# Kernel tuning notes

Hardware: AMD Instinct MI355X
Metric: run time of the kernel (lower is better)

The kernel has to match this reference:

```python
import jax, jax.numpy as jnp
import numpy as np

N, E, IN, HID, H, OUT = 50000, 800000, 128, 64, 4, 128
NEG = 0.2   # LeakyReLU slope in GATv2
EPS = 1e-5  # BatchNorm eps


def _seg_softmax(a, seg, n):
    # numerically stable softmax over edges grouped by destination node
    amax = jax.lax.stop_gradient(jax.ops.segment_max(a, seg, num_segments=n))
    amax = jnp.where(jnp.isfinite(amax), amax, 0.0)
    ex = jnp.exp(a - amax[seg])
    den = jax.ops.segment_sum(ex, seg, num_segments=n)
    return ex / (den[seg] + 1e-16)


def _gatv2(x, src, dst, e_attr, Wl, bl, Wr, br, We, att, bias, heads, c, concat):
    n = x.shape[0]
    xl = (x @ Wl + bl).reshape(n, heads, c)   # source transform (x_j)
    xr = (x @ Wr + br).reshape(n, heads, c)   # target transform (x_i)
    ee = (e_attr @ We).reshape(-1, heads, c)  # edge feature transform
    m = xl[src] + xr[dst] + ee                # [E, H, C]
    m = jnp.where(m > 0, m, NEG * m)          # LeakyReLU
    alpha = _seg_softmax(jnp.einsum('ehc,hc->eh', m, att), dst, n)  # [E, H]
    out = jax.ops.segment_sum(alpha[:, :, None] * xl[src], dst, num_segments=n)
    out = out.reshape(n, heads * c) if concat else out.mean(axis=1)
    return out + bias


def _bn(h, g, b):  # BatchNorm1d, training-mode batch stats (biased var)
    mu = jnp.mean(h, axis=0)
    var = jnp.var(h, axis=0)
    return (h - mu) * jax.lax.rsqrt(var + EPS) * g + b


def _prelu(h, a):
    return jnp.where(h > 0, h, a * h)


def setup_inputs() -> dict:
    key = jax.random.key(0)
    ks = jax.random.split(key, 16)
    def nrm(k, shape, fan):
        return jax.random.normal(k, shape, jnp.float32) / np.float32(np.sqrt(fan))
    x = jax.random.normal(ks[0], (N, IN), jnp.float32)
    edge_index = jax.random.randint(ks[1], (2, E), 0, N, jnp.int32)
    edge_attr = jax.random.uniform(ks[2], (E, 1), dtype=jnp.float32)
    return {
        'x': x, 'edge_index': edge_index, 'edge_attr': edge_attr,
        # layer 1: heads=4, concat=True
        'Wl1': nrm(ks[3], (IN, H * HID), IN), 'bl1': jnp.zeros((H * HID,), jnp.float32),
        'Wr1': nrm(ks[4], (IN, H * HID), IN), 'br1': jnp.zeros((H * HID,), jnp.float32),
        'We1': nrm(ks[5], (1, H * HID), 1),
        'att1': nrm(ks[6], (H, HID), HID),
        'cb1': jnp.zeros((H * HID,), jnp.float32),
        'bng1': jnp.ones((H * HID,), jnp.float32), 'bnb1': jnp.zeros((H * HID,), jnp.float32),
        'pa': jnp.float32(0.25),  # PReLU single parameter (shared by both uses)
        # layer 2: heads=1, concat=False
        'Wl2': nrm(ks[7], (H * HID, OUT), H * HID), 'bl2': jnp.zeros((OUT,), jnp.float32),
        'Wr2': nrm(ks[8], (H * HID, OUT), H * HID), 'br2': jnp.zeros((OUT,), jnp.float32),
        'We2': nrm(ks[9], (1, OUT), 1),
        'att2': nrm(ks[10], (1, OUT), OUT),
        'cb2': jnp.zeros((OUT,), jnp.float32),
        'bng2': jnp.ones((OUT,), jnp.float32), 'bnb2': jnp.zeros((OUT,), jnp.float32),
        'skipW': nrm(ks[11], (IN, OUT), IN), 'skipb': jnp.zeros((OUT,), jnp.float32),
    }


def reference(x, edge_index, edge_attr, Wl1, bl1, Wr1, br1, We1, att1, cb1,
              bng1, bnb1, pa, Wl2, bl2, Wr2, br2, We2, att2, cb2, bng2, bnb2,
              skipW, skipb):
    src, dst = edge_index[0], edge_index[1]
    h = _gatv2(x, src, dst, edge_attr, Wl1, bl1, Wr1, br1, We1, att1, cb1, H, HID, True)
    h = _prelu(_bn(h, bng1, bnb1), pa)  # dropout = identity (eval)
    h = _gatv2(h, src, dst, edge_attr, Wl2, bl2, Wr2, br2, We2, att2, cb2, 1, OUT, False)
    h = _prelu(_bn(h, bng2, bnb2), pa)
    return h + (x @ skipW + skipb)
```

## Files before the change

kernel.cpp:

```cpp
#include <hip/hip_runtime.h>
#include <cstdint>
#include <cstddef>

#define NNODES 50000
#define NEDGES 800000
#define DH1    256
#define DOUT   128

typedef unsigned short u16;
typedef __bf16 bf16x8 __attribute__((ext_vector_type(8)));
typedef float  f32x4  __attribute__((ext_vector_type(4)));

__device__ __forceinline__ float bf2f(unsigned int u) {
  union { unsigned int i; float f; } x; x.i = u << 16; return x.f;
}
__device__ __forceinline__ u16 f2bf(float f) {
  union { float f; unsigned int i; } x; x.f = f;
  unsigned int r = x.i + 0x7fffu + ((x.i >> 16) & 1u);
  return (u16)(r >> 16);
}
__device__ __forceinline__ void dec8(uint4 r, float* o) {
  o[0] = bf2f(r.x & 0xffffu); o[1] = bf2f(r.x >> 16);
  o[2] = bf2f(r.y & 0xffffu); o[3] = bf2f(r.y >> 16);
  o[4] = bf2f(r.z & 0xffffu); o[5] = bf2f(r.z >> 16);
  o[6] = bf2f(r.w & 0xffffu); o[7] = bf2f(r.w >> 16);
}
__device__ __forceinline__ uint4 pack8(const float* v) {
  uint4 p;
  p.x = (unsigned)f2bf(v[0]) | ((unsigned)f2bf(v[1]) << 16);
  p.y = (unsigned)f2bf(v[2]) | ((unsigned)f2bf(v[3]) << 16);
  p.z = (unsigned)f2bf(v[4]) | ((unsigned)f2bf(v[5]) << 16);
  p.w = (unsigned)f2bf(v[6]) | ((unsigned)f2bf(v[7]) << 16);
  return p;
}
template<int IMM>
__device__ __forceinline__ float swz(float v) {
  return __int_as_float(__builtin_amdgcn_ds_swizzle(__float_as_int(v), IMM));
}


#define CNT_BLKS 3125
#define CVT_BLKS 6250
#define W1_BLKS  320
#define W2_BLKS  256

__global__ __launch_bounds__(256) void setup_k(
    const int* __restrict__ dst, int* __restrict__ cnt, int* __restrict__ rank,
    const float* __restrict__ x, u16* __restrict__ xbf,
    const float* __restrict__ Wl1, const float* __restrict__ Wr1,
    const float* __restrict__ bl1, const float* __restrict__ br1,
    const float* __restrict__ Wl2, const float* __restrict__ Wr2,
    const float* __restrict__ bl2, const float* __restrict__ br2,
    const float* __restrict__ skW, const float* __restrict__ skb,
    const float* __restrict__ att1, const float* __restrict__ We1,
    const float* __restrict__ att2, const float* __restrict__ We2,
    u16* __restrict__ Wcat1, float* __restrict__ bias1,
    u16* __restrict__ Wt2, float* __restrict__ bias2,
    float* __restrict__ axw, int2* __restrict__ epair) {
  int b = blockIdx.x, t = threadIdx.x;
  if (b < CNT_BLKS) {
    int e = b * 256 + t;
    if (e < NEDGES) rank[e] = atomicAdd(&cnt[dst[e]], 1);
  } else if (b < CNT_BLKS + CVT_BLKS) {
    int i = ((b - CNT_BLKS) * 256 + t) * 4;
    float4 v = *reinterpret_cast<const float4*>(x + i);
    uint2 pk;
    pk.x = (unsigned)f2bf(v.x) | ((unsigned)f2bf(v.y) << 16);
    pk.y = (unsigned)f2bf(v.z) | ((unsigned)f2bf(v.w) << 16);
    *reinterpret_cast<uint2*>(xbf + i) = pk;
  } else if (b < CNT_BLKS + CVT_BLKS + W1_BLKS) {
    int idx = (b - CNT_BLKS - CVT_BLKS) * 256 + t;
    if (idx < 640) bias1[idx] = idx < 256 ? bl1[idx] : idx < 512 ? br1[idx - 256] : skb[idx - 512];
    int n = idx >> 7, k = idx & 127;
    float v = n < 256 ? Wl1[k * 256 + n] : n < 512 ? Wr1[k * 256 + (n - 256)] : skW[k * 128 + (n - 512)];
    Wcat1[idx] = f2bf(v);
  } else if (b < CNT_BLKS + CVT_BLKS + W1_BLKS + W2_BLKS) {
    int idx = (b - CNT_BLKS - CVT_BLKS - W1_BLKS) * 256 + t;
    if (idx < 256) bias2[idx] = idx < 128 ? bl2[idx] : br2[idx - 128];
    int n = idx >> 8, k = idx & 255;
    float v = n < 128 ? Wl2[k * 128 + n] : Wr2[k * 128 + (n - 128)];
    Wt2[idx] = f2bf(v);
  } else if (b == CNT_BLKS + CVT_BLKS + W1_BLKS + W2_BLKS) {
    if (t < 4) {
      float s = 0.f;
      for (int c = 0; c < 64; ++c) s += att1[t * 64 + c] * We1[t * 64 + c];
      axw[t] = s;
    } else if (t == 4) {
      float s = 0.f;
      for (int c = 0; c < 128; ++c) s += att2[c] * We2[c];
      axw[4] = s;
    }
  } else {
    int2 z; z.x = 0; z.y = 0;
    epair[NEDGES + t] = z;
  }
}


__global__ __launch_bounds__(256) void offsets_k(const int* __restrict__ cnt, int* __restrict__ offs,
                                                 int* __restrict__ total) {
  int i = blockIdx.x * 256 + threadIdx.x;
  int lane = threadIdx.x & 63;
  int c = (i < NNODES) ? cnt[i] : 0;
  int incl = c;
  #pragma unroll
  for (int d = 1; d < 64; d <<= 1) {
    int t = __shfl_up(incl, d, 64);
    if (lane >= d) incl += t;
  }
  int wtotal = __shfl(incl, 63, 64);
  int base = 0;
  if (lane == 63) base = atomicAdd(total, wtotal);
  base = __shfl(base, 63, 64);
  int off = base + incl - c;
  if (i < NNODES) offs[i] = off;
}

__global__ __launch_bounds__(256) void scatter_k(const int* __restrict__ src, const int* __restrict__ dst,
                                                 const float* __restrict__ ea, const int* __restrict__ offs,
                                                 const int* __restrict__ rank, int2* __restrict__ epair) {
  int e = blockIdx.x * 256 + threadIdx.x;
  if (e >= NEDGES) return;
  int p = offs[dst[e]] + rank[e];
  int2 v; v.x = src[e]; v.y = __float_as_int(ea[e]);
  epair[p] = v;
}


template<int K, int NPASS, int B1, int B2, int LDC0, int LDC1, int LDC2,
         int SPAN, int ATTLEN, bool DO_ATT, bool FUSE_BN>
__global__ __launch_bounds__(512) void gemm_fused(
    const u16* __restrict__ A, const u16* __restrict__ Wt, const float* __restrict__ bias,
    u16* __restrict__ C0, u16* __restrict__ C1, u16* __restrict__ C2,
    const float* __restrict__ att, float* __restrict__ axl, float* __restrict__ axr,
    const float* __restrict__ bnsum, const float* __restrict__ bnsq,
    const float* __restrict__ bng, const float* __restrict__ bnb,
    const float* __restrict__ pap) {
  constexpr int LDA = K + 8;
  constexpr int CSTR = 136;
  __shared__ __align__(16) u16 As[64 * LDA];
  __shared__ __align__(16) u16 Cs[64 * CSTR];
  __shared__ float attS[128];
  __shared__ float scS[K], shS[K];
  const int tid = threadIdx.x;
  const int row0 = blockIdx.x * 64;

  if constexpr (FUSE_BN) {
    if (tid < K) {
      const float invN = 1.0f / (float)NNODES;
      float mu = bnsum[tid] * invN;
      float var = bnsq[tid] * invN - mu * mu;
      float s = bng[tid] * rsqrtf(var + 1e-5f);
      scS[tid] = s;
      shS[tid] = bnb[tid] - mu * s;
    }
    __syncthreads();
  }
  const float pa = FUSE_BN ? pap[0] : 0.f;
  #pragma unroll
  for (int it = 0; it < K / 32; ++it) {
    int chunk = it * 512 + tid;
    int row = chunk / (K / 4);
    int col = (chunk % (K / 4)) * 4;
    uint2 v; v.x = 0u; v.y = 0u;
    int gr = row0 + row;
    if (gr < NNODES) v = *reinterpret_cast<const uint2*>(A + (size_t)gr * K + col);
    if constexpr (FUSE_BN) {
      float o0 = bf2f(v.x & 0xffffu) * scS[col]     + shS[col];
      float o1 = bf2f(v.x >> 16)     * scS[col + 1] + shS[col + 1];
      float o2 = bf2f(v.y & 0xffffu) * scS[col + 2] + shS[col + 2];
      float o3 = bf2f(v.y >> 16)     * scS[col + 3] + shS[col + 3];
      o0 = o0 > 0.f ? o0 : pa * o0;
      o1 = o1 > 0.f ? o1 : pa * o1;
      o2 = o2 > 0.f ? o2 : pa * o2;
      o3 = o3 > 0.f ? o3 : pa * o3;
      v.x = (unsigned)f2bf(o0) | ((unsigned)f2bf(o1) << 16);
      v.y = (unsigned)f2bf(o2) | ((unsigned)f2bf(o3) << 16);
    }
    *reinterpret_cast<uint2*>(&As[row * LDA + col]) = v;
  }
  __syncthreads();

  const int w = tid >> 6, lane = tid & 63, q = lane >> 4, l16 = lane & 15;
  const int tc = w * 16 + l16;

  #pragma unroll
  for (int p = 0; p < NPASS; ++p) {
    const int cb = p * 128;
    const int ncol = cb + tc;
    f32x4 acc[4];
    #pragma unroll
    for (int rt = 0; rt < 4; ++rt) acc[rt] = (f32x4){0.f, 0.f, 0.f, 0.f};
    const u16* wp = Wt + (size_t)ncol * K + q * 8;
    #pragma unroll
    for (int ks = 0; ks < K / 32; ++ks) {
      bf16x8 b = *reinterpret_cast<const bf16x8*>(wp + ks * 32);
      #pragma unroll
      for (int rt = 0; rt < 4; ++rt) {
        bf16x8 a = *reinterpret_cast<const bf16x8*>(&As[(rt * 16 + l16) * LDA + ks * 32 + q * 8]);
        acc[rt] = __builtin_amdgcn_mfma_f32_16x16x32_bf16(a, b, acc[rt], 0, 0, 0);
      }
    }
    const float bval = bias[ncol];
    #pragma unroll
    for (int rt = 0; rt < 4; ++rt)
      #pragma unroll
      for (int r = 0; r < 4; ++r)
        Cs[(rt * 16 + q * 4 + r) * CSTR + tc] = f2bf(acc[rt][r] + bval);
    if (DO_ATT && cb < B2 && tid < 128) attS[tid] = att[(cb + tid) % ATTLEN];
    __syncthreads();
    {
      u16* Cg; int LD, cc;
      if (cb < B1)      { Cg = C0; LD = LDC0; cc = cb; }
      else if (cb < B2) { Cg = C1; LD = LDC1; cc = cb - B1; }
      else              { Cg = C2; LD = LDC2; cc = cb - B2; }
      #pragma unroll
      for (int it = 0; it < 2; ++it) {
        int ch = it * 512 + tid;
        int row = ch / 16, co = (ch % 16) * 8;
        int grow = row0 + row;
        if (grow < NNODES) {
          uint4 v = *reinterpret_cast<const uint4*>(&Cs[row * CSTR + co]);
          *reinterpret_cast<uint4*>(Cg + (size_t)grow * LD + cc + co) = v;
        }
      }
    }
    if constexpr (DO_ATT) {
      if (cb < B2) {
        constexpr int TPU = SPAN / 16;
        constexpr int HIT = 128 / SPAN;
        constexpr int HEADS = B1 / SPAN;
        int unit = tid / TPU, sub = tid % TPU;
        int row = unit / HIT, hb = unit % HIT;
        int c0 = hb * SPAN + sub * 16;
        float s = 0.f;
        #pragma unroll
        for (int c = 0; c < 16; ++c)
          s += bf2f(Cs[row * CSTR + c0 + c]) * attS[c0 + c];
        #pragma unroll
        for (int d = 1; d < TPU; d <<= 1) s += __shfl_xor(s, d, 64);
        int grow = row0 + row;
        if (sub == 0 && grow < NNODES) {
          int cbl = cb < B1 ? cb : cb - B1;
          int head = cbl / SPAN + hb;
          float* dstp = (cb < B1) ? axl : axr;
          dstp[grow * HEADS + head] = s;
        }
      }
    }
    __syncthreads();
  }
}


template<int HEADS, int CHAN, int EPW>
__global__ __launch_bounds__(256) void gat_edge(
    const int* __restrict__ offs, const int* __restrict__ cnt,
    const int2* __restrict__ epair,
    const u16* __restrict__ xl, const u16* __restrict__ xr,
    const float* __restrict__ att, const float* __restrict__ We,
    const float* __restrict__ cb,
    const float* __restrict__ axl, const float* __restrict__ axr,
    const float* __restrict__ aWep, u16* __restrict__ hout) {
  constexpr int HC  = HEADS * CHAN;
  constexpr int GSZ = 64 / EPW;
  constexpr int CPL = HC / GSZ;
  constexpr int LPH = CHAN / CPL;
  static_assert(CPL == 8, "layout");

  int node = __builtin_amdgcn_readfirstlane((int)(blockIdx.x * 4 + (threadIdx.x >> 6)));
  if (node >= NNODES) return;
  const int lane = threadIdx.x & 63;
  const int g    = lane / GSZ;
  const int lgs  = lane & (GSZ - 1);
  const int h    = lgs / LPH;
  const int cbase = lgs * CPL;

  float xrv[8], attv[8], wev[8];
  {
    uint4 xrr = *reinterpret_cast<const uint4*>(xr + (size_t)node * HC + cbase);
    dec8(xrr, xrv);
    float4 a0 = *reinterpret_cast<const float4*>(att + cbase);
    float4 a1 = *reinterpret_cast<const float4*>(att + cbase + 4);
    float4 w0 = *reinterpret_cast<const float4*>(We + cbase);
    float4 w1 = *reinterpret_cast<const float4*>(We + cbase + 4);
    attv[0]=a0.x; attv[1]=a0.y; attv[2]=a0.z; attv[3]=a0.w;
    attv[4]=a1.x; attv[5]=a1.y; attv[6]=a1.z; attv[7]=a1.w;
    wev[0]=w0.x; wev[1]=w0.y; wev[2]=w0.z; wev[3]=w0.w;
    wev[4]=w1.x; wev[5]=w1.y; wev[6]=w1.z; wev[7]=w1.w;
  }
  const float aWe = aWep[h];
  const float axr_n = axr[node * HEADS + h];
  const int off = __builtin_amdgcn_readfirstlane(offs[node]);
  const int deg = __builtin_amdgcn_readfirstlane(cnt[node]);

  float den = 0.f;
  float accv[8];
  #pragma unroll
  for (int c = 0; c < 8; ++c) accv[c] = 0.f;

  {
    const int last = deg - 1;
    const int2* pp = epair + off + g;
    int2 p_cur = pp[0];
    int2 p_nxt = pp[EPW];
    uint4 r_cur; float ax_cur;
    { int s = p_cur.x;
      r_cur = *reinterpret_cast<const uint4*>(xl + (size_t)s * HC + cbase);
      ax_cur = axl[s * HEADS + h]; }
    const int niter = (deg + EPW - 1) / EPW;
    for (int i = 0; i < niter; ++i) {
      int2 p_n2 = pp[(i + 2) * EPW];
      uint4 r_n; float ax_n;
      { int s = p_nxt.x;
        r_n = *reinterpret_cast<const uint4*>(xl + (size_t)s * HC + cbase);
        ax_n = axl[s * HEADS + h]; }
      float ea = __int_as_float(p_cur.y);
      float xlv[8];
      dec8(r_cur, xlv);
      float part2 = 0.f;
      #pragma unroll
      for (int c = 0; c < 8; ++c) {
        float m = xlv[c] + fmaf(ea, wev[c], xrv[c]);
        part2 = fmaf(fabsf(m), attv[c], part2);
      }
      if constexpr (LPH >= 2)  part2 += swz<0x041F>(part2);
      if constexpr (LPH >= 4)  part2 += swz<0x081F>(part2);
      if constexpr (LPH >= 8)  part2 += swz<0x101F>(part2);
      if constexpr (LPH >= 16) part2 += swz<0x201F>(part2);
      float ssum = ax_cur + fmaf(ea, aWe, axr_n);
      float sc = fmaf(0.4f, part2, 0.6f * ssum);
      float e = __expf(sc);
      e = (i * EPW + g <= last) ? e : 0.f;
      den += e;
      #pragma unroll
      for (int c = 0; c < 8; ++c) accv[c] = fmaf(e, xlv[c], accv[c]);
      p_cur = p_nxt; p_nxt = p_n2; r_cur = r_n; ax_cur = ax_n;
    }
  }
  #pragma unroll
  for (int d = GSZ; d < 64; d <<= 1) {
    den += __shfl_xor(den, d, 64);
    #pragma unroll
    for (int c = 0; c < 8; ++c) accv[c] += __shfl_xor(accv[c], d, 64);
  }
  if (g == 0) {
    float inv = 1.0f / (den + 1e-16f);
    float4 c0 = *reinterpret_cast<const float4*>(cb + cbase);
    float4 c1 = *reinterpret_cast<const float4*>(cb + cbase + 4);
    float ov[8];
    ov[0] = accv[0] * inv + c0.x; ov[1] = accv[1] * inv + c0.y;
    ov[2] = accv[2] * inv + c0.z; ov[3] = accv[3] * inv + c0.w;
    ov[4] = accv[4] * inv + c1.x; ov[5] = accv[5] * inv + c1.y;
    ov[6] = accv[6] * inv + c1.z; ov[7] = accv[7] * inv + c1.w;
    *reinterpret_cast<uint4*>(hout + (size_t)node * HC + cbase) = pack8(ov);
  }
}


template<int NC>
__global__ void bn_stats_bf(const u16* __restrict__ h, float* __restrict__ sum, float* __restrict__ sq) {
  int c = threadIdx.x;
  float s = 0.f, q = 0.f;
  for (int r = blockIdx.x; r < NNODES; r += gridDim.x) {
    float v = bf2f(h[(size_t)r * NC + c]);
    s += v; q += v * v;
  }
  atomicAdd(&sum[c], s);
  atomicAdd(&sq[c], q);
}

__global__ __launch_bounds__(256) void final_out_k(
    const u16* __restrict__ h2, const u16* __restrict__ skip,
    const float* __restrict__ sum, const float* __restrict__ sq,
    const float* __restrict__ g, const float* __restrict__ bb_,
    const float* __restrict__ pap, float* __restrict__ outp, int total) {
  int i = (blockIdx.x * 256 + threadIdx.x) * 4;
  if (i >= total) return;
  const float invN = 1.0f / (float)NNODES;
  float pa = pap[0];
  int c = i & 127;
  float4 sm = *reinterpret_cast<const float4*>(sum + c);
  float4 qq = *reinterpret_cast<const float4*>(sq + c);
  float4 gg = *reinterpret_cast<const float4*>(g + c);
  float4 bb = *reinterpret_cast<const float4*>(bb_ + c);
  float mu, var, sc[4], sh[4];
  mu = sm.x * invN; var = qq.x * invN - mu * mu; sc[0] = gg.x * rsqrtf(var + 1e-5f); sh[0] = bb.x - mu * sc[0];
  mu = sm.y * invN; var = qq.y * invN - mu * mu; sc[1] = gg.y * rsqrtf(var + 1e-5f); sh[1] = bb.y - mu * sc[1];
  mu = sm.z * invN; var = qq.z * invN - mu * mu; sc[2] = gg.z * rsqrtf(var + 1e-5f); sh[2] = bb.z - mu * sc[2];
  mu = sm.w * invN; var = qq.w * invN - mu * mu; sc[3] = gg.w * rsqrtf(var + 1e-5f); sh[3] = bb.w - mu * sc[3];
  uint2 raw = *reinterpret_cast<const uint2*>(h2 + i);
  float v0 = bf2f(raw.x & 0xffffu), v1 = bf2f(raw.x >> 16);
  float v2 = bf2f(raw.y & 0xffffu), v3 = bf2f(raw.y >> 16);
  uint2 skr = *reinterpret_cast<const uint2*>(skip + i);
  float s0 = bf2f(skr.x & 0xffffu), s1 = bf2f(skr.x >> 16);
  float s2 = bf2f(skr.y & 0xffffu), s3 = bf2f(skr.y >> 16);
  float4 o;
  o.x = v0 * sc[0] + sh[0]; o.x = (o.x > 0.f ? o.x : pa * o.x) + s0;
  o.y = v1 * sc[1] + sh[1]; o.y = (o.y > 0.f ? o.y : pa * o.y) + s1;
  o.z = v2 * sc[2] + sh[2]; o.z = (o.z > 0.f ? o.z : pa * o.z) + s2;
  o.w = v3 * sc[3] + sh[3]; o.w = (o.w > 0.f ? o.w : pa * o.w) + s3;
  *reinterpret_cast<float4*>(outp + i) = o;
}


extern "C" void kernel_launch(void* const* d_in, const int* in_sizes, int n_in,
                              void* d_out, int out_size, void* d_ws, size_t ws_size,
                              hipStream_t stream) {
  (void)in_sizes; (void)n_in; (void)out_size; (void)ws_size;
  const float* x    = (const float*)d_in[0];
  const int*   ei   = (const int*)d_in[1];
  const float* ea   = (const float*)d_in[2];
  const float* Wl1  = (const float*)d_in[3];
  const float* bl1  = (const float*)d_in[4];
  const float* Wr1  = (const float*)d_in[5];
  const float* br1  = (const float*)d_in[6];
  const float* We1  = (const float*)d_in[7];
  const float* att1 = (const float*)d_in[8];
  const float* cb1  = (const float*)d_in[9];
  const float* bng1 = (const float*)d_in[10];
  const float* bnb1 = (const float*)d_in[11];
  const float* pa   = (const float*)d_in[12];
  const float* Wl2  = (const float*)d_in[13];
  const float* bl2  = (const float*)d_in[14];
  const float* Wr2  = (const float*)d_in[15];
  const float* br2  = (const float*)d_in[16];
  const float* We2  = (const float*)d_in[17];
  const float* att2 = (const float*)d_in[18];
  const float* cb2  = (const float*)d_in[19];
  const float* bng2 = (const float*)d_in[20];
  const float* bnb2 = (const float*)d_in[21];
  const float* skW  = (const float*)d_in[22];
  const float* skb  = (const float*)d_in[23];
  const int* srcp = ei;
  const int* dstp = ei + NEDGES;

  char* base = (char*)d_ws;
  size_t off = 0;
  auto alloc = [&](size_t bytes) -> char* {
    char* p = base + off;
    off = (off + bytes + 255) & ~(size_t)255;
    return p;
  };
  size_t zero_ints = 1 + NNODES + 256 + 256 + 128 + 128;
  char* zbase = alloc(zero_ints * 4);
  int*   totalp = (int*)zbase;
  int*   cnt    = totalp + 1;
  float* bnsum1 = (float*)(cnt + NNODES);
  float* bnsq1  = bnsum1 + 256;
  float* bnsum2 = bnsq1 + 256;
  float* bnsq2  = bnsum2 + 128;

  int*   offs    = (int*)alloc((size_t)NNODES * 4);
  int*   rank    = (int*)alloc((size_t)NEDGES * 4);
  int2*  epair   = (int2*)alloc(((size_t)NEDGES + 256) * 8);
  const size_t RBYTES = (size_t)NNODES * DH1 * 2;
  char* regionA = alloc(RBYTES);
  char* regionB = alloc(RBYTES);
  char* regionC = alloc(RBYTES);
  u16*   xbf    = (u16*)alloc((size_t)NNODES * 128 * 2);
  u16*   skipbf = (u16*)alloc((size_t)NNODES * 128 * 2);
  u16*   Wcat1  = (u16*)alloc(640 * 128 * 2);
  u16*   Wt2    = (u16*)alloc(256 * 256 * 2);
  float* bias1  = (float*)alloc(640 * 4);
  float* bias2  = (float*)alloc(256 * 4);
  float* axw    = (float*)alloc(8 * 4);
  float* axl1   = (float*)alloc((size_t)NNODES * 4 * 4);
  float* axr1   = (float*)alloc((size_t)NNODES * 4 * 4);
  float* axl2   = (float*)alloc((size_t)NNODES * 4);
  float* axr2   = (float*)alloc((size_t)NNODES * 4);

  u16*   xl1     = (u16*)regionA;
  u16*   xr1     = (u16*)regionB;
  u16*   h1      = (u16*)regionC;
  u16*   xl2     = (u16*)regionB;
  u16*   xr2     = (u16*)(regionB + (size_t)NNODES * DOUT * 2);
  u16*   h2      = (u16*)regionA;

  hipMemsetAsync(zbase, 0, zero_ints * 4, stream);

  const int EB = (NEDGES + 255) / 256;
  const int NB = (NNODES + 255) / 256;
  setup_k<<<CNT_BLKS + CVT_BLKS + W1_BLKS + W2_BLKS + 2, 256, 0, stream>>>(
      dstp, cnt, rank, x, xbf, Wl1, Wr1, bl1, br1, Wl2, Wr2, bl2, br2, skW, skb,
      att1, We1, att2, We2, Wcat1, bias1, Wt2, bias2, axw, epair);
  offsets_k<<<NB, 256, 0, stream>>>(cnt, offs, totalp);
  scatter_k<<<EB, 256, 0, stream>>>(srcp, dstp, ea, offs, rank, epair);

  const int MB64 = (NNODES + 63) / 64;
  gemm_fused<128, 5, 256, 512, 256, 256, 128, 64, 256, true, false><<<MB64, 512, 0, stream>>>(
      xbf, Wcat1, bias1, xl1, xr1, skipbf, att1, axl1, axr1,
      (const float*)0, (const float*)0, (const float*)0, (const float*)0, (const float*)0);
  gat_edge<4, 64, 2><<<(NNODES + 3) / 4, 256, 0, stream>>>(
      offs, cnt, epair, xl1, xr1, att1, We1, cb1, axl1, axr1, axw, h1);
  bn_stats_bf<256><<<800, 256, 0, stream>>>(h1, bnsum1, bnsq1);

  gemm_fused<256, 2, 128, 256, 128, 128, 1, 128, 128, true, true><<<MB64, 512, 0, stream>>>(
      h1, Wt2, bias2, xl2, xr2, (u16*)0, att2, axl2, axr2,
      bnsum1, bnsq1, bng1, bnb1, pa);
  gat_edge<1, 128, 4><<<(NNODES + 3) / 4, 256, 0, stream>>>(
      offs, cnt, epair, xl2, xr2, att2, We2, cb2, axl2, axr2, axw + 4, h2);
  bn_stats_bf<128><<<800, 128, 0, stream>>>(h2, bnsum2, bnsq2);
  final_out_k<<<(NNODES * DOUT / 4 + 255) / 256, 256, 0, stream>>>(
      h2, skipbf, bnsum2, bnsq2, bng2, bnb2, pa, (float*)d_out, NNODES * DOUT);
}
```

Baseline: 447.2 us.

## Fold softmax constants into exp2, use DPP reductions, deepen edge prefetch

The 0.6·log2(e) and 0.4·log2(e) factors of the rewritten LeakyReLU score are now folded into the precomputed axl/axr/axw values and the attention vector. The edge loop can then call a raw exp2 with no extra multiplies. The cross-lane partial-sum reduction switches from ds_swizzle to DPP adds, which avoids the LDS-path latency. Source-row gathers are prefetched two edges ahead instead of one, using 32-bit byte offsets, and the tail mask is checked only on the last iteration. The deeper prefetch costs extra registers.

After: 439.5 us. About the same (-1.7%).

```diff
diff --git a/kernel.cpp b/kernel.cpp
--- a/kernel.cpp
+++ b/kernel.cpp
@@ -6,6 +6,9 @@
 #define NEDGES 800000
 #define DH1    256
 #define DOUT   128
+
+#define K1F 0.8656170245333781f
+#define K2F 0.5770780163555854f
 
 typedef unsigned short u16;
 typedef __bf16 bf16x8 __attribute__((ext_vector_type(8)));
@@ -33,9 +36,17 @@
   p.w = (unsigned)f2bf(v[6]) | ((unsigned)f2bf(v[7]) << 16);
   return p;
 }
-template<int IMM>
-__device__ __forceinline__ float swz(float v) {
-  return __int_as_float(__builtin_amdgcn_ds_swizzle(__float_as_int(v), IMM));
+template<int CTRL>
+__device__ __forceinline__ float dppadd(float v) {
+  int t = __builtin_amdgcn_update_dpp(0, __float_as_int(v), CTRL, 0xF, 0xF, true);
+  return v + __int_as_float(t);
+}
+__device__ __forceinline__ float fexp2(float x) {
+#if __has_builtin(__builtin_amdgcn_exp2f)
+  return __builtin_amdgcn_exp2f(x);
+#else
+  return exp2f(x);
+#endif
 }
 
 
@@ -84,11 +95,11 @@
     if (t < 4) {
       float s = 0.f;
       for (int c = 0; c < 64; ++c) s += att1[t * 64 + c] * We1[t * 64 + c];
-      axw[t] = s;
+      axw[t] = s * K1F;
     } else if (t == 4) {
       float s = 0.f;
       for (int c = 0; c < 128; ++c) s += att2[c] * We2[c];
-      axw[4] = s;
+      axw[4] = s * K1F;
     }
   } else {
     int2 z; z.x = 0; z.y = 0;
@@ -244,7 +255,7 @@
           int cbl = cb < B1 ? cb : cb - B1;
           int head = cbl / SPAN + hb;
           float* dstp = (cb < B1) ? axl : axr;
-          dstp[grow * HEADS + head] = s;
+          dstp[grow * HEADS + head] = s * K1F;
         }
       }
     }
@@ -284,8 +295,8 @@
     float4 a1 = *reinterpret_cast<const float4*>(att + cbase + 4);
     float4 w0 = *reinterpret_cast<const float4*>(We + cbase);
     float4 w1 = *reinterpret_cast<const float4*>(We + cbase + 4);
-    attv[0]=a0.x; attv[1]=a0.y; attv[2]=a0.z; attv[3]=a0.w;
-    attv[4]=a1.x; attv[5]=a1.y; attv[6]=a1.z; attv[7]=a1.w;
+    attv[0]=a0.x*K2F; attv[1]=a0.y*K2F; attv[2]=a0.z*K2F; attv[3]=a0.w*K2F;
+    attv[4]=a1.x*K2F; attv[5]=a1.y*K2F; attv[6]=a1.z*K2F; attv[7]=a1.w*K2F;
     wev[0]=w0.x; wev[1]=w0.y; wev[2]=w0.z; wev[3]=w0.w;
     wev[4]=w1.x; wev[5]=w1.y; wev[6]=w1.z; wev[7]=w1.w;
   }
@@ -294,49 +305,58 @@
   const int off = __builtin_amdgcn_readfirstlane(offs[node]);
   const int deg = __builtin_amdgcn_readfirstlane(cnt[node]);
 
+  const char* __restrict__ xlb  = (const char*)xl;
+  const char* __restrict__ axlb = (const char*)axl;
+  const unsigned cboff = (unsigned)(cbase * 2);
+  const unsigned hoff  = (unsigned)(h * 4);
+
   float den = 0.f;
   float accv[8];
   #pragma unroll
   for (int c = 0; c < 8; ++c) accv[c] = 0.f;
 
+  const int niter = (deg + EPW - 1) / EPW;
+  const int2* pp = epair + off + g;
+  int2 p0 = pp[0];
+  int2 p1 = pp[EPW];
+  int2 p2 = pp[2 * EPW];
+  uint4 r0, r1; float ax0, ax1;
   {
-    const int last = deg - 1;
-    const int2* pp = epair + off + g;
-    int2 p_cur = pp[0];
-    int2 p_nxt = pp[EPW];
-    uint4 r_cur; float ax_cur;
-    { int s = p_cur.x;
-      r_cur = *reinterpret_cast<const uint4*>(xl + (size_t)s * HC + cbase);
-      ax_cur = axl[s * HEADS + h]; }
-    const int niter = (deg + EPW - 1) / EPW;
-    for (int i = 0; i < niter; ++i) {
-      int2 p_n2 = pp[(i + 2) * EPW];
-      uint4 r_n; float ax_n;
-      { int s = p_nxt.x;
-        r_n = *reinterpret_cast<const uint4*>(xl + (size_t)s * HC + cbase);
-        ax_n = axl[s * HEADS + h]; }
-      float ea = __int_as_float(p_cur.y);
-      float xlv[8];
-      dec8(r_cur, xlv);
-      float part2 = 0.f;
-      #pragma unroll
-      for (int c = 0; c < 8; ++c) {
-        float m = xlv[c] + fmaf(ea, wev[c], xrv[c]);
-        part2 = fmaf(fabsf(m), attv[c], part2);
-      }
-      if constexpr (LPH >= 2)  part2 += swz<0x041F>(part2);
-      if constexpr (LPH >= 4)  part2 += swz<0x081F>(part2);
-      if constexpr (LPH >= 8)  part2 += swz<0x101F>(part2);
-      if constexpr (LPH >= 16) part2 += swz<0x201F>(part2);
-      float ssum = ax_cur + fmaf(ea, aWe, axr_n);
-      float sc = fmaf(0.4f, part2, 0.6f * ssum);
-      float e = __expf(sc);
-      e = (i * EPW + g <= last) ? e : 0.f;
-      den += e;
-      #pragma unroll
-      for (int c = 0; c < 8; ++c) accv[c] = fmaf(e, xlv[c], accv[c]);
-      p_cur = p_nxt; p_nxt = p_n2; r_cur = r_n; ax_cur = ax_n;
-    }
+    unsigned b0 = (unsigned)p0.x * (unsigned)(HC * 2) + cboff;
+    r0  = *reinterpret_cast<const uint4*>(xlb + b0);
+    ax0 = *reinterpret_cast<const float*>(axlb + ((unsigned)p0.x * (unsigned)(HEADS * 4) + hoff));
+    unsigned b1 = (unsigned)p1.x * (unsigned)(HC * 2) + cboff;
+    r1  = *reinterpret_cast<const uint4*>(xlb + b1);
+    ax1 = *reinterpret_cast<const float*>(axlb + ((unsigned)p1.x * (unsigned)(HEADS * 4) + hoff));
+  }
+  const int lastg = deg - 1 - (niter - 1) * EPW;
+  for (int i = 0; i < niter; ++i) {
+    int2 p3 = pp[(i + 3) * EPW];
+    uint4 r2; float ax2;
+    {
+      unsigned b2 = (unsigned)p2.x * (unsigned)(HC * 2) + cboff;
+      r2  = *reinterpret_cast<const uint4*>(xlb + b2);
+      ax2 = *reinterpret_cast<const float*>(axlb + ((unsigned)p2.x * (unsigned)(HEADS * 4) + hoff));
+    }
+    float ea = __int_as_float(p0.y);
+    float xlv[8];
+    dec8(r0, xlv);
+    float part2 = 0.f;
+    #pragma unroll
+    for (int c = 0; c < 8; ++c) {
+      float m = xlv[c] + fmaf(ea, wev[c], xrv[c]);
+      part2 = fmaf(fabsf(m), attv[c], part2);
+    }
+    if constexpr (LPH >= 2)  part2 = dppadd<0xB1>(part2);
+    if constexpr (LPH >= 4)  part2 = dppadd<0x4E>(part2);
+    if constexpr (LPH >= 8)  part2 = dppadd<0x141>(part2);
+    if constexpr (LPH >= 16) part2 = dppadd<0x140>(part2);
+    float e = fexp2(part2 + fmaf(ea, aWe, axr_n) + ax0);
+    if (i == niter - 1) e = (g <= lastg) ? e : 0.f;
+    den += e;
+    #pragma unroll
+    for (int c = 0; c < 8; ++c) accv[c] = fmaf(e, xlv[c], accv[c]);
+    p0 = p1; p1 = p2; p2 = p3; r0 = r1; r1 = r2; ax0 = ax1; ax1 = ax2;
   }
   #pragma unroll
   for (int d = GSZ; d < 64; d <<= 1) {
```
